# Kernel optimization log

Hardware: AMD Instinct MI355X
Metric: run time of the kernel (lower is better)

The kernel has to match this reference:

```python
import jax, jax.numpy as jnp
import numpy as np

GRID = 1024  # grid resolution -> V = GRID*GRID vertices


def _grid_mesh(G):
    """Build a triangulated GxG grid mesh; return laplacian directed edges and
    normal-consistency interior-edge index quadruples [v0, v1, v2, v3] where
    (v0,v1) is the shared edge and v2, v3 the opposite vertices of the two faces."""
    V = G * G
    i, j = np.meshgrid(np.arange(G - 1), np.arange(G - 1), indexing="ij")
    a = (i * G + j).ravel(); b = (i * G + j + 1).ravel()
    c = ((i + 1) * G + j).ravel(); d = ((i + 1) * G + j + 1).ravel()
    faces = np.concatenate([np.stack([a, b, c], 1), np.stack([b, d, c], 1)], 0).astype(np.int64)
    # half-edges with opposite vertex per face
    e = np.concatenate([faces[:, [0, 1]], faces[:, [1, 2]], faces[:, [2, 0]]], 0)
    opp = np.concatenate([faces[:, 2], faces[:, 0], faces[:, 1]], 0)
    e = np.sort(e, 1)
    key = e[:, 0] * V + e[:, 1]
    order = np.argsort(key, kind="stable")
    ks, opps = key[order], opp[order]
    dup = np.nonzero(ks[1:] == ks[:-1])[0]  # edges shared by exactly two faces
    nc_idx = np.stack([ks[dup] // V, ks[dup] % V, opps[dup], opps[dup + 1]], 1)
    uk = np.unique(key)
    src, dst = uk // V, uk % V
    lap_src = np.concatenate([src, dst])
    lap_dst = np.concatenate([dst, src])
    return lap_src.astype(np.int32), lap_dst.astype(np.int32), nc_idx.astype(np.int32)


def setup_inputs() -> dict:
    key = jax.random.key(0)
    k1, k2 = jax.random.split(key)
    G = GRID; V = G * G
    lap_src, lap_dst, nc_idx = _grid_mesh(G)
    verts = jax.random.normal(k1, (V, 3), jnp.float32)          # template_mesh.verts_packed()
    deform_verts = jax.random.normal(k2, (V, 3), jnp.float32) * 0.05  # nn.Parameter
    return {
        "verts": verts,
        "deform_verts": deform_verts,
        "lap_src": jnp.asarray(lap_src),
        "lap_dst": jnp.asarray(lap_dst),
        "nc_idx": jnp.asarray(nc_idx),
        "batch_size": 4,
    }


def reference(verts, deform_verts, lap_src, lap_dst, nc_idx, batch_size):
    V = verts.shape[0]
    new_verts = verts + deform_verts  # Meshes.offset_verts

    # mesh_laplacian_smoothing(method='uniform'):
    # per-vertex (mean of neighbors - vertex), loss = mean ||.||
    nbr_sum = jax.ops.segment_sum(new_verts[lap_src], lap_dst, num_segments=V)
    deg = jax.ops.segment_sum(jnp.ones(lap_src.shape, jnp.float32), lap_dst, num_segments=V)
    lap = nbr_sum / jnp.maximum(deg, 1.0)[:, None] - new_verts
    laplacian_loss = jnp.linalg.norm(lap, axis=1).mean()

    # mesh_normal_consistency: for each interior edge (v0,v1) with opposite
    # verts v2, v3: n0 = (v1-v0) x (v2-v0), n1 = -(v1-v0) x (v3-v0),
    # loss = mean(1 - cos(n0, n1))
    v0 = new_verts[nc_idx[:, 0]]; v1 = new_verts[nc_idx[:, 1]]
    v2 = new_verts[nc_idx[:, 2]]; v3 = new_verts[nc_idx[:, 3]]
    e01 = v1 - v0
    n0 = jnp.cross(e01, v2 - v0)
    n1 = -jnp.cross(e01, v3 - v0)
    cos = (n0 * n1).sum(-1) / jnp.maximum(
        jnp.linalg.norm(n0, axis=-1) * jnp.linalg.norm(n1, axis=-1), 1e-8)
    flatten_loss = (1.0 - cos).mean()

    # Meshes.extend(batch_size): replicate deformed mesh verts
    batched_verts = jnp.broadcast_to(new_verts, (batch_size, V, 3))
    return batched_verts, laplacian_loss, flatten_loss
```

## Files before the change

### kernel.cpp

```cpp
#include <hip/hip_runtime.h>

#define G 1024
#define ROWF 3072
#define ROWF4 768
#define V (G * G)
#define NBLK 1024
#define COPY4 786432
#define NEDGE 3137541.0f

typedef float v4 __attribute__((ext_vector_type(4)));

struct F3 { float x, y, z; };

__device__ inline float frcp(float x) { return __builtin_amdgcn_rcpf(x); }

__device__ inline F3 ldl(const float* __restrict__ nv, int slot, int col) {
    int b = slot * ROWF + 3 * col;
    F3 r; r.x = nv[b]; r.y = nv[b + 1]; r.z = nv[b + 2];
    return r;
}

__device__ inline float omc(F3 v0, F3 v1, F3 v2, F3 v3) {
    float ex = v1.x - v0.x, ey = v1.y - v0.y, ez = v1.z - v0.z;
    float ax = v2.x - v0.x, ay = v2.y - v0.y, az = v2.z - v0.z;
    float bx = v3.x - v0.x, by = v3.y - v0.y, bz = v3.z - v0.z;
    float n0x = ey * az - ez * ay;
    float n0y = ez * ax - ex * az;
    float n0z = ex * ay - ey * ax;
    float n1x = ez * by - ey * bz;
    float n1y = ex * bz - ez * bx;
    float n1z = ey * bx - ex * by;
    float dd  = n0x * n1x + n0y * n1y + n0z * n1z;
    float q   = (n0x * n0x + n0y * n0y + n0z * n0z)
    float c   = dd * frcp(fmaxf(sqrtf(q), 1e-8f));
    return 1.0f - c;
}

__global__ __launch_bounds__(256) void fused_kernel(const float* __restrict__ verts,
                                                    const float* __restrict__ dv,
                                                    float* __restrict__ out,
                                                    float* __restrict__ wsp) {
    int b = blockIdx.x;
    int i = ((b & 7) << 7) | (b >> 3);
    int t = threadIdx.x;

    __shared__ v4 nv4[3 * ROWF4];
    const float* nv = (const float*)nv4;

    const v4* vin4 = (const v4*)verts;
    const v4* dvi4 = (const v4*)dv;
    v4* out4 = (v4*)out;

    #pragma unroll
    for (int s = 0; s < 3; ++s) {
        int r = i + s - 1;
        r = r < 0 ? 0 : (r > G - 1 ? G - 1 : r);
        int base = r * ROWF4;
        #pragma unroll
        for (int k = 0; k < 3; ++k) {
            int idx = t + (k << 8);
            v4 val  = vin4[base + idx] + dvi4[base + idx];
            nv4[s * ROWF4 + idx] = val;
            if (s == 1) {
                int oi = base + idx;
                __builtin_nontemporal_store(val, &out4[oi]);
                __builtin_nontemporal_store(val, &out4[oi + COPY4]);
                __builtin_nontemporal_store(val, &out4[oi + 2 * COPY4]);
                __builtin_nontemporal_store(val, &out4[oi + 3 * COPY4]);
            }
        }
    }
    __syncthreads();

    bool hasU = (i > 0), hasD = (i < G - 1);

    float lap_sum = 0.0f, fl_sum = 0.0f;

    #pragma unroll
    for (int k = 0; k < 4; ++k) {
        int j = t + (k << 8);
        bool hasL = (j > 0), hasR = (j < G - 1);

        F3 self = ldl(nv, 1, j);
        F3 pL{0,0,0}, pR{0,0,0}, pU{0,0,0}, pD{0,0,0}, pUR{0,0,0}, pDL{0,0,0}, pDR{0,0,0};
        if (hasL)          pL  = ldl(nv, 1, j - 1);
        if (hasR)          pR  = ldl(nv, 1, j + 1);
        if (hasU)          pU  = ldl(nv, 0, j);
        if (hasD)          pD  = ldl(nv, 2, j);
        if (hasU && hasR)  pUR = ldl(nv, 0, j + 1);
        if (hasD && hasL)  pDL = ldl(nv, 2, j - 1);
        if (hasD && hasR)  pDR = ldl(nv, 2, j + 1);

        int   degi = (int)hasL + (int)hasR + (int)hasU + (int)hasD
                   + (int)(hasU && hasR) + (int)(hasD && hasL);
        float inv  = frcp((float)degi);
        float lx = (pL.x + pR.x + pU.x + pD.x + pUR.x + pDL.x) * inv - self.x;
        float ly = (pL.y + pR.y + pU.y + pD.y + pUR.y + pDL.y) * inv - self.y;
        float lz = (pL.z + pR.z + pU.z + pD.z + pUR.z + pDL.z) * inv - self.z;
        lap_sum += sqrtf(lx * lx + ly * ly + lz * lz);

        if (hasD && hasR) {
            fl_sum += omc(pR, pD, self, pDR);
            if (hasU) fl_sum += omc(self, pR, pD, pUR);
            if (hasL) fl_sum += omc(self, pD, pR, pDL);
        }
    }

    for (int off = 32; off > 0; off >>= 1) {
        lap_sum += __shfl_down(lap_sum, off);
        fl_sum  += __shfl_down(fl_sum, off);
    }
    __shared__ float red[8];
    int lane = t & 63, wv = t >> 6;
    if (lane == 0) { red[wv] = lap_sum; red[4 + wv] = fl_sum; }
    __syncthreads();
    if (t == 0) {
        wsp[b]        = red[0] + red[1] + red[2] + red[3];
        wsp[NBLK + b] = red[4] + red[5] + red[6] + red[7];
    }
}

__global__ __launch_bounds__(256) void finalize_kernel(const float* __restrict__ wsp,
                                                       float* __restrict__ out) {
    float s = 0.0f, f = 0.0f;
    for (int k = threadIdx.x; k < NBLK; k += 256) {
        s += wsp[k];
        f += wsp[NBLK + k];
    }
    for (int off = 32; off > 0; off >>= 1) {
        s += __shfl_down(s, off);
        f += __shfl_down(f, off);
    }
    __shared__ float red[8];
    int lane = threadIdx.x & 63, wv = threadIdx.x >> 6;
    if (lane == 0) { red[wv] = s; red[4 + wv] = f; }
    __syncthreads();
    if (threadIdx.x == 0) {
        out[12 * V]     = (red[0] + red[1] + red[2] + red[3]) / (float)V;
        out[12 * V + 1] = (red[4] + red[5] + red[6] + red[7]) / NEDGE;
    }
}

extern "C" void kernel_launch(void* const* d_in, const int* in_sizes, int n_in,
                              void* d_out, int out_size, void* d_ws, size_t ws_size,
                              hipStream_t stream) {
    const float* verts = (const float*)d_in[0];
    const float* dv    = (const float*)d_in[1];
    float* out = (float*)d_out;
    float* wsp = (float*)d_ws;

    fused_kernel<<<NBLK, 256, 0, stream>>>(verts, dv, out, wsp);
    finalize_kernel<<<1, 256, 0, stream>>>(wsp, out);
}
```

Before: 155.5 us.

## Split each grid row across two blocks with halo segments in shared memory

Each row is now handled by two blocks, each taking half the columns, so the grid doubles to 2048 blocks. Each block loads only a 385-float4 segment per stencil row, including a halo, into a smaller LDS tile and writes out only its own 384 float4s. Launch bounds ask for 8 blocks per CU. This aims to improve occupancy and load balance across CUs, at the cost of redundant halo loads and more index arithmetic.

```diff
diff --git a/kernel.cpp b/kernel.cpp
--- a/kernel.cpp
+++ b/kernel.cpp
@@ -1,11 +1,12 @@
 #include <hip/hip_runtime.h>
 
 #define G 1024
-#define ROWF 3072
 #define ROWF4 768
 #define V (G * G)
-#define NBLK 1024
+#define NBLK 2048
 #define COPY4 786432
+#define SEG 385
+#define SEGP 388
 #define NEDGE 3137541.0f
 
 typedef float v4 __attribute__((ext_vector_type(4)));
@@ -14,8 +15,8 @@
 
 __device__ inline float frcp(float x) { return __builtin_amdgcn_rcpf(x); }
 
-__device__ inline F3 ldl(const float* __restrict__ nv, int slot, int col) {
-    int b = slot * ROWF + 3 * col;
+__device__ inline F3 ldl(const float* __restrict__ nv, int slot, int fo) {
+    int b = slot * (SEGP * 4) + fo;
     F3 r; r.x = nv[b]; r.y = nv[b + 1]; r.z = nv[b + 2];
     return r;
 }
@@ -36,20 +37,26 @@
     return 1.0f - c;
 }
 
-__global__ __launch_bounds__(256) void fused_kernel(const float* __restrict__ verts,
-                                                    const float* __restrict__ dv,
-                                                    float* __restrict__ out,
-                                                    float* __restrict__ wsp) {
-    int b = blockIdx.x;
-    int i = ((b & 7) << 7) | (b >> 3);
-    int t = threadIdx.x;
+__global__ __launch_bounds__(256, 8) void fused_kernel(const float* __restrict__ verts,
+                                                       const float* __restrict__ dv,
+                                                       float* __restrict__ out,
+                                                       float* __restrict__ wsp) {
+    int b  = blockIdx.x;
+    int m  = b >> 3;
+    int i  = (((b & 7) << 7) | (m >> 1));
+    int h  = m & 1;
+    int t  = threadIdx.x;
 
-    __shared__ v4 nv4[3 * ROWF4];
+    int S = h ? 383 : 0;
+
+    __shared__ v4 nv4[3 * SEGP];
     const float* nv = (const float*)nv4;
 
     const v4* vin4 = (const v4*)verts;
     const v4* dvi4 = (const v4*)dv;
     v4* out4 = (v4*)out;
+
+    int ownS = h * 384;
 
     #pragma unroll
     for (int s = 0; s < 3; ++s) {
@@ -57,16 +64,19 @@
         r = r < 0 ? 0 : (r > G - 1 ? G - 1 : r);
         int base = r * ROWF4;
         #pragma unroll
-        for (int k = 0; k < 3; ++k) {
-            int idx = t + (k << 8);
-            v4 val  = vin4[base + idx] + dvi4[base + idx];
-            nv4[s * ROWF4 + idx] = val;
-            if (s == 1) {
-                int oi = base + idx;
-                __builtin_nontemporal_store(val, &out4[oi]);
-                __builtin_nontemporal_store(val, &out4[oi + COPY4]);
-                __builtin_nontemporal_store(val, &out4[oi + 2 * COPY4]);
-                __builtin_nontemporal_store(val, &out4[oi + 3 * COPY4]);
+        for (int m2 = 0; m2 < 2; ++m2) {
+            int idx = t + (m2 << 8);
+            if (idx < SEG) {
+                int gf4 = S + idx;
+                v4 val  = vin4[base + gf4] + dvi4[base + gf4];
+                nv4[s * SEGP + idx] = val;
+                if (s == 1 && gf4 >= ownS && gf4 < ownS + 384) {
+                    int oi = i * ROWF4 + gf4;
+                    __builtin_nontemporal_store(val, &out4[oi]);
+                    __builtin_nontemporal_store(val, &out4[oi + COPY4]);
+                    __builtin_nontemporal_store(val, &out4[oi + 2 * COPY4]);
+                    __builtin_nontemporal_store(val, &out4[oi + 3 * COPY4]);
+                }
             }
         }
     }
@@ -77,19 +87,20 @@
     float lap_sum = 0.0f, fl_sum = 0.0f;
 
     #pragma unroll
-    for (int k = 0; k < 4; ++k) {
-        int j = t + (k << 8);
+    for (int k = 0; k < 2; ++k) {
+        int j  = (h << 9) + t + (k << 8);
+        int fo = 3 * j - 4 * S;
         bool hasL = (j > 0), hasR = (j < G - 1);
 
-        F3 self = ldl(nv, 1, j);
+        F3 self = ldl(nv, 1, fo);
         F3 pL{0,0,0}, pR{0,0,0}, pU{0,0,0}, pD{0,0,0}, pUR{0,0,0}, pDL{0,0,0}, pDR{0,0,0};
-        if (hasL)          pL  = ldl(nv, 1, j - 1);
-        if (hasR)          pR  = ldl(nv, 1, j + 1);
-        if (hasU)          pU  = ldl(nv, 0, j);
-        if (hasD)          pD  = ldl(nv, 2, j);
-        if (hasU && hasR)  pUR = ldl(nv, 0, j + 1);
-        if (hasD && hasL)  pDL = ldl(nv, 2, j - 1);
-        if (hasD && hasR)  pDR = ldl(nv, 2, j + 1);
+        if (hasL)          pL  = ldl(nv, 1, fo - 3);
+        if (hasR)          pR  = ldl(nv, 1, fo + 3);
+        if (hasU)          pU  = ldl(nv, 0, fo);
+        if (hasD)          pD  = ldl(nv, 2, fo);
+        if (hasU && hasR)  pUR = ldl(nv, 0, fo + 3);
+        if (hasD && hasL)  pDL = ldl(nv, 2, fo - 3);
+        if (hasD && hasR)  pDR = ldl(nv, 2, fo + 3);
 
         int   degi = (int)hasL + (int)hasR + (int)hasU + (int)hasD
                    + (int)(hasU && hasR) + (int)(hasD && hasL);
```

After: 169.1 us. 8.8% more time.

## Replace shared-memory row staging with register rows and wavefront shuffles

Applied to the files above, without the earlier changes.

Each thread now loads three contiguous float4s (4 vertices) per row directly into registers for the current, upper and lower rows. Horizontal neighbours come from cross-lane shuffles, with extra global loads at wave edges, so the LDS buffer and its barrier go away. Replicated output stores switch from nontemporal to regular stores, and launch bounds now request 4 blocks per SM. The cost is higher register pressure, extra halo loads, and possibly worse cache behaviour for the 4x output copy.

```diff
diff --git a/kernel.cpp b/kernel.cpp
--- a/kernel.cpp
+++ b/kernel.cpp
@@ -1,7 +1,6 @@
 #include <hip/hip_runtime.h>
 
 #define G 1024
-#define ROWF 3072
 #define ROWF4 768
 #define V (G * G)
 #define NBLK 1024
@@ -12,12 +11,51 @@
 
 struct F3 { float x, y, z; };
 
+struct Row {
+    float v[12];
+    float lf[3];
+    float rt[3];
+};
+
 __device__ inline float frcp(float x) { return __builtin_amdgcn_rcpf(x); }
 
-__device__ inline F3 ldl(const float* __restrict__ nv, int slot, int col) {
-    int b = slot * ROWF + 3 * col;
-    F3 r; r.x = nv[b]; r.y = nv[b + 1]; r.z = nv[b + 2];
-    return r;
+__device__ inline F3 at(const float* p, int q) { F3 r; r.x = p[3*q]; r.y = p[3*q+1]; r.z = p[3*q+2]; return r; }
+__device__ inline F3 f3(const float* p)        { F3 r; r.x = p[0];   r.y = p[1];     r.z = p[2];     return r; }
+
+template <bool STORE>
+__device__ inline void load_row(const v4* __restrict__ vin4, const v4* __restrict__ dvi4,
+                                v4* __restrict__ out4, int r, int w, int l, Row& R) {
+    int base = r * ROWF4 + 192 * w + 3 * l;
+    v4 a = vin4[base]     + dvi4[base];
+    v4 b = vin4[base + 1] + dvi4[base + 1];
+    v4 c = vin4[base + 2] + dvi4[base + 2];
+    R.v[0] = a.x; R.v[1] = a.y; R.v[2]  = a.z; R.v[3]  = a.w;
+    R.v[4] = b.x; R.v[5] = b.y; R.v[6]  = b.z; R.v[7]  = b.w;
+    R.v[8] = c.x; R.v[9] = c.y; R.v[10] = c.z; R.v[11] = c.w;
+
+    if (STORE) {
+        int ob = base;
+        out4[ob] = a;              out4[ob + 1] = b;              out4[ob + 2] = c;
+        out4[ob + COPY4] = a;      out4[ob + COPY4 + 1] = b;      out4[ob + COPY4 + 2] = c;
+        out4[ob + 2*COPY4] = a;    out4[ob + 2*COPY4 + 1] = b;    out4[ob + 2*COPY4 + 2] = c;
+        out4[ob + 3*COPY4] = a;    out4[ob + 3*COPY4 + 1] = b;    out4[ob + 3*COPY4 + 2] = c;
+    }
+
+    R.lf[0] = __shfl_up(R.v[9], 1);  R.lf[1] = __shfl_up(R.v[10], 1); R.lf[2] = __shfl_up(R.v[11], 1);
+    R.rt[0] = __shfl_down(R.v[0], 1); R.rt[1] = __shfl_down(R.v[1], 1); R.rt[2] = __shfl_down(R.v[2], 1);
+
+    if (l == 0) {
+        int g = r * ROWF4 + 192 * w - 1;
+        g = g < 0 ? 0 : g;
+        v4 h = vin4[g] + dvi4[g];
+        R.lf[0] = h.y; R.lf[1] = h.z; R.lf[2] = h.w;
+    }
+    if (l == 63) {
+        int g = r * ROWF4 + 192 * w + 192;
+        g = g > G * ROWF4 - 1 ? G * ROWF4 - 1 : g;
+        v4 h = vin4[g] + dvi4[g];
+        R.rt[0] = h.x; R.rt[1] = h.y; R.rt[2] = h.z;
+    }
 }
 
 __device__ inline float omc(F3 v0, F3 v1, F3 v2, F3 v3) {
@@ -36,60 +74,45 @@
     return 1.0f - c;
 }
 
-__global__ __launch_bounds__(256) void fused_kernel(const float* __restrict__ verts,
-                                                    const float* __restrict__ dv,
-                                                    float* __restrict__ out,
-                                                    float* __restrict__ wsp) {
+__global__ __launch_bounds__(256, 4) void fused_kernel(const float* __restrict__ verts,
+                                                       const float* __restrict__ dv,
+                                                       float* __restrict__ out,
+                                                       float* __restrict__ wsp) {
     int b = blockIdx.x;
     int i = ((b & 7) << 7) | (b >> 3);
     int t = threadIdx.x;
-
-    __shared__ v4 nv4[3 * ROWF4];
-    const float* nv = (const float*)nv4;
+    int w = t >> 6, l = t & 63;
+    int c0 = (w << 8) + (l << 2);
 
     const v4* vin4 = (const v4*)verts;
     const v4* dvi4 = (const v4*)dv;
     v4* out4 = (v4*)out;
 
-    #pragma unroll
-    for (int s = 0; s < 3; ++s) {
-        int r = i + s - 1;
-        r = r < 0 ? 0 : (r > G - 1 ? G - 1 : r);
-        int base = r * ROWF4;
-        #pragma unroll
-        for (int k = 0; k < 3; ++k) {
-            int idx = t + (k << 8);
-            v4 val  = vin4[base + idx] + dvi4[base + idx];
-            nv4[s * ROWF4 + idx] = val;
-            if (s == 1) {
-                int oi = base + idx;
-                __builtin_nontemporal_store(val, &out4[oi]);
-                __builtin_nontemporal_store(val, &out4[oi + COPY4]);
-                __builtin_nontemporal_store(val, &out4[oi + 2 * COPY4]);
-                __builtin_nontemporal_store(val, &out4[oi + 3 * COPY4]);
-            }
-        }
-    }
-    __syncthreads();
+    bool hasU = (i > 0), hasD = (i < G - 1);
 
-    bool hasU = (i > 0), hasD = (i < G - 1);
+    Row S, U = {}, D = {};
+    load_row<true>(vin4, dvi4, out4, i, w, l, S);
+    if (hasU) load_row<false>(vin4, dvi4, out4, i - 1, w, l, U);
+    if (hasD) load_row<false>(vin4, dvi4, out4, i + 1, w, l, D);
 
     float lap_sum = 0.0f, fl_sum = 0.0f;
 
     #pragma unroll
-    for (int k = 0; k < 4; ++k) {
-        int j = t + (k << 8);
+    for (int q = 0; q < 4; ++q) {
+        int j = c0 + q;
         bool hasL = (j > 0), hasR = (j < G - 1);
 
-        F3 self = ldl(nv, 1, j);
-        F3 pL{0,0,0}, pR{0,0,0}, pU{0,0,0}, pD{0,0,0}, pUR{0,0,0}, pDL{0,0,0}, pDR{0,0,0};
-        if (hasL)          pL  = ldl(nv, 1, j - 1);
-        if (hasR)          pR  = ldl(nv, 1, j + 1);
-        if (hasU)          pU  = ldl(nv, 0, j);
-        if (hasD)          pD  = ldl(nv, 2, j);
-        if (hasU && hasR)  pUR = ldl(nv, 0, j + 1);
-        if (hasD && hasL)  pDL = ldl(nv, 2, j - 1);
-        if (hasD && hasR)  pDR = ldl(nv, 2, j + 1);
+        F3 self = at(S.v, q);
+        F3 pL  = (q == 0) ? f3(S.lf) : at(S.v, q - 1);
+        F3 pR  = (q == 3) ? f3(S.rt) : at(S.v, q + 1);
+        F3 pU  = at(U.v, q);
+        F3 pD  = at(D.v, q);
+        F3 pUR = (q == 3) ? f3(U.rt) : at(U.v, q + 1);
+        F3 pDL = (q == 0) ? f3(D.lf) : at(D.v, q - 1);
+        F3 pDR = (q == 3) ? f3(D.rt) : at(D.v, q + 1);
+        if (!hasL) { pL.x = pL.y = pL.z = 0.0f; pDL.x = pDL.y = pDL.z = 0.0f; }
+        if (!hasR) { pR.x = pR.y = pR.z = 0.0f; pUR.x = pUR.y = pUR.z = 0.0f;
+                     pDR.x = pDR.y = pDR.z = 0.0f; }
 
         int   degi = (int)hasL + (int)hasR + (int)hasU + (int)hasD
                    + (int)(hasU && hasR) + (int)(hasD && hasL);
@@ -111,8 +134,7 @@
         fl_sum  += __shfl_down(fl_sum, off);
     }
     __shared__ float red[8];
-    int lane = t & 63, wv = t >> 6;
-    if (lane == 0) { red[wv] = lap_sum; red[4 + wv] = fl_sum; }
+    if (l == 0) { red[w] = lap_sum; red[4 + w] = fl_sum; }
     __syncthreads();
     if (t == 0) {
         wsp[b]        = red[0] + red[1] + red[2] + red[3];
```

After: 161.2 us. 3.7% more time.
